# Kernel tuning notes

Measured on AMD Instinct MI355X. Metric: run time of the kernel, lower is better.

## Reference

```python
import jax, jax.numpy as jnp
import numpy as np

N = 100000
E = 1600000
IN_C, HID_C, OUT_C = 128, 64, 32


def _add_self_loops(edge_index, n):
    loops = jnp.arange(n, dtype=edge_index.dtype)
    src = jnp.concatenate([edge_index[0], loops])
    dst = jnp.concatenate([edge_index[1], loops])
    return src, dst


def _gcn_norm(src, dst, n):
    # symmetric normalization on A + I with unit edge weights
    deg = jax.ops.segment_sum(jnp.ones_like(dst, dtype=jnp.float32), dst, num_segments=n)
    dinv = jnp.where(deg > 0, jax.lax.rsqrt(deg), 0.0)
    return dinv[src] * dinv[dst]  # [E+N]


def _gcn_conv(x, src, dst, norm, W, b, n):
    h = x @ W                              # [N, out]
    msg = h[src] * norm[:, None]           # [E+N, out]  (dominant gather)
    out = jax.ops.segment_sum(msg, dst, num_segments=n)
    return out + b


def setup_inputs() -> dict:
    key = jax.random.key(0)
    k = jax.random.split(key, 6)
    x = jax.random.normal(k[0], (N, IN_C), dtype=jnp.float32)
    edge_index = jax.random.randint(k[1], (2, E), 0, N, dtype=jnp.int32)
    # Glorot-style init for GCN weights
    W1 = jax.random.normal(k[2], (IN_C, HID_C), dtype=jnp.float32) / np.sqrt(IN_C)
    b1 = jnp.zeros((HID_C,), dtype=jnp.float32)
    W2 = jax.random.normal(k[3], (HID_C, OUT_C), dtype=jnp.float32) / np.sqrt(HID_C)
    b2 = jnp.zeros((OUT_C,), dtype=jnp.float32)
    return {"x": x, "edge_index": edge_index, "W1": W1, "b1": b1, "W2": W2, "b2": b2}


def reference(x, edge_index, W1, b1, W2, b2):
    src, dst = _add_self_loops(edge_index, N)
    norm = _gcn_norm(src, dst, N)
    h = _gcn_conv(x, src, dst, norm, W1, b1, N)
    h = jax.nn.relu(h)
    # dropout p=0.2 is identity in eval mode
    out = _gcn_conv(h, src, dst, norm, W2, b2, N)
    return out
```

## Files before the change

kernel.cpp:

```cpp
#include <hip/hip_runtime.h>
#include <hip/hip_fp16.h>

#define N_NODES 100000
#define E_EDGES 1600000
#define IN_C 128
#define HID_C 64
#define OUT_C 32
#define BNODES 64
#define NBUCK ((N_NODES + BNODES - 1) / BNODES)
#define MAXB 2048
#define NCHUNK 256
#define CHUNK_E (E_EDGES / NCHUNK)
#define SCAN_N (NBUCK * NCHUNK)
#define SCAN_NB (SCAN_N / 256)

__device__ __forceinline__ int chunk_of_block(int b) { return (b & 7) * (NCHUNK / 8) + (b >> 3); }

__global__ __launch_bounds__(1024) void chunk_hist_kernel(const int* __restrict__ dst,
                                                          int* __restrict__ hist) {
    __shared__ int h[NBUCK];
    for (int i = threadIdx.x; i < NBUCK; i += 1024) h[i] = 0;
    __syncthreads();
    const int chunk = chunk_of_block(blockIdx.x);
    const int base = chunk * CHUNK_E;
    for (int j = threadIdx.x; j < CHUNK_E; j += 1024)
        atomicAdd(&h[dst[base + j] >> 6], 1);
    __syncthreads();
    for (int i = threadIdx.x; i < NBUCK; i += 1024)
        hist[i * NCHUNK + chunk] = h[i];
}

__global__ void scan1_kernel(int* __restrict__ data, int* __restrict__ bsums) {
    __shared__ int s[256];
    int i = blockIdx.x * 256 + threadIdx.x;
    int v = data[i];
    s[threadIdx.x] = v;
    __syncthreads();
    for (int off = 1; off < 256; off <<= 1) {
        int t = (threadIdx.x >= off) ? s[threadIdx.x - off] : 0;
        __syncthreads();
        s[threadIdx.x] += t;
        __syncthreads();
    }
    data[i] = s[threadIdx.x] - v;
    if (threadIdx.x == 255) bsums[blockIdx.x] = s[255];
}

__global__ __launch_bounds__(1024) void scan2_kernel(int* __restrict__ bsums) {
    __shared__ int s[1024];
    int total = 0;
    for (int base = 0; base < SCAN_NB; base += 1024) {
        int i = base + threadIdx.x;
        int v = (i < SCAN_NB) ? bsums[i] : 0;
        s[threadIdx.x] = v;
        __syncthreads();
        for (int off = 1; off < 1024; off <<= 1) {
            int t = (threadIdx.x >= off) ? s[threadIdx.x - off] : 0;
            __syncthreads();
            s[threadIdx.x] += t;
            __syncthreads();
        }
        if (i < SCAN_NB) bsums[i] = total + s[threadIdx.x] - v;
        total += s[1023];
        __syncthreads();
    }
}

__global__ __launch_bounds__(1024) void chunk_fill_kernel(const int* __restrict__ src,
                                                          const int* __restrict__ dst,
                                                          const int* __restrict__ hist,
                                                          const int* __restrict__ bsums,
                                                          unsigned* __restrict__ pairs) {
    __shared__ int cur[NBUCK];
    const int chunk = chunk_of_block(blockIdx.x);
    for (int i = threadIdx.x; i < NBUCK; i += 1024)
        cur[i] = hist[i * NCHUNK + chunk] + bsums[i];
    __syncthreads();
    const int base = chunk * CHUNK_E;
    for (int j = threadIdx.x; j < CHUNK_E; j += 1024) {
        int d = dst[base + j];
        int pos = atomicAdd(&cur[d >> 6], 1);
        pairs[pos] = ((unsigned)src[base + j] << 6) | (unsigned)(d & 63);
    }
}

__global__ __launch_bounds__(256) void bucket_sort_kernel(const int* __restrict__ hist,
                                                          const int* __restrict__ bsums,
                                                          unsigned* __restrict__ pairs,
                                                          int* __restrict__ row_ptr,
                                                          float* __restrict__ dinv) {
    __shared__ unsigned sp[MAXB];
    __shared__ int hcnt[BNODES], scn[BNODES], cur[BNODES];
    const int b = blockIdx.x;
    const int beg = hist[b * NCHUNK] + bsums[b];
    const int end = (b + 1 < NBUCK) ? hist[(b + 1) * NCHUNK] + bsums[b + 1] : E_EDGES;
    const int cnt = end - beg;
    if (threadIdx.x < BNODES) hcnt[threadIdx.x] = 0;
    __syncthreads();
    for (int j = threadIdx.x; j < cnt; j += 256) {
        unsigned p = pairs[beg + j];
        sp[j] = p;
        atomicAdd(&hcnt[p & 63], 1);
    }
    __syncthreads();
    if (threadIdx.x < BNODES) scn[threadIdx.x] = hcnt[threadIdx.x];
    __syncthreads();
    for (int off = 1; off < BNODES; off <<= 1) {
        int t = 0;
        if (threadIdx.x < BNODES && threadIdx.x >= off) t = scn[threadIdx.x - off];
        __syncthreads();
        if (threadIdx.x < BNODES) scn[threadIdx.x] += t;
        __syncthreads();
    }
    if (threadIdx.x < BNODES) {
        int ex = scn[threadIdx.x] - hcnt[threadIdx.x];
        cur[threadIdx.x] = ex;
        int node = b * BNODES + threadIdx.x;
        if (node < N_NODES) {
            row_ptr[node] = beg + ex;
            dinv[node] = rsqrtf((float)hcnt[threadIdx.x] + 1.0f);
        }
    }
    if (threadIdx.x == 0 && b == NBUCK - 1) row_ptr[N_NODES] = E_EDGES;
    __syncthreads();
    for (int j = threadIdx.x; j < cnt; j += 256) {
        unsigned p = sp[j];
        int pos = atomicAdd(&cur[p & 63], 1);
        pairs[beg + pos] = p >> 6;
    }
}

__global__ __launch_bounds__(256) void gemm1_kernel(const float* __restrict__ x,
                                                    const float* __restrict__ W1,
                                                    const float* __restrict__ dinv,
                                                    __half* __restrict__ hs) {
    __shared__ float sW[IN_C * HID_C];
    for (int i = threadIdx.x; i < IN_C * HID_C; i += 256) sW[i] = W1[i];
    __syncthreads();
    const int cg = (threadIdx.x & 7) * 8;
    const int row0 = blockIdx.x * 128 + (threadIdx.x >> 3) * 4;
    float acc[4][8];
#pragma unroll
    for (int r = 0; r < 4; ++r)
#pragma unroll
        for (int c = 0; c < 8; ++c) acc[r][c] = 0.f;

    int rr[4];
#pragma unroll
    for (int r = 0; r < 4; ++r) rr[r] = min(row0 + r, N_NODES - 1);

    const float4* x4 = (const float4*)x;
#pragma unroll 2
    for (int k4 = 0; k4 < IN_C / 4; ++k4) {
        float4 xv[4];
#pragma unroll
        for (int r = 0; r < 4; ++r) xv[r] = x4[(size_t)rr[r] * (IN_C / 4) + k4];
        float xs[4][4];
#pragma unroll
        for (int r = 0; r < 4; ++r) {
            xs[r][0] = xv[r].x; xs[r][1] = xv[r].y; xs[r][2] = xv[r].z; xs[r][3] = xv[r].w;
        }
#pragma unroll
        for (int kk = 0; kk < 4; ++kk) {
            const float4* wp = (const float4*)(sW + (k4 * 4 + kk) * HID_C + cg);
            float4 w0 = wp[0], w1 = wp[1];
            float wv[8] = {w0.x, w0.y, w0.z, w0.w, w1.x, w1.y, w1.z, w1.w};
#pragma unroll
            for (int r = 0; r < 4; ++r)
#pragma unroll
                for (int c = 0; c < 8; ++c)
                    acc[r][c] = fmaf(xs[r][kk], wv[c], acc[r][c]);
        }
    }
#pragma unroll
    for (int r = 0; r < 4; ++r) {
        int row = row0 + r;
        if (row < N_NODES) {
            float dv = dinv[row];
            union { float4 f; __half2 h[4]; } u;
#pragma unroll
            for (int q = 0; q < 4; ++q)
                u.h[q] = __floats2half2_rn(acc[r][2 * q] * dv, acc[r][2 * q + 1] * dv);
            *(float4*)(hs + (size_t)row * HID_C + cg) = u.f;
        }
    }
}

__global__ void agg1_kernel(const int* __restrict__ row_ptr, const int* __restrict__ col,
                            const __half2* __restrict__ hs2, const float* __restrict__ dinv,
                            const float* __restrict__ b1, __half2* __restrict__ h2h) {
    const int node = blockIdx.x * 8 + (threadIdx.x >> 5);
    const int c2 = threadIdx.x & 31;
    if (node >= N_NODES) return;
    const int beg = row_ptr[node], end = row_ptr[node + 1];
    float2 f = __half22float2(hs2[node * 32 + c2]);
    float ax = f.x, ay = f.y;
    int j = beg;
    for (; j + 7 < end; j += 8) {
        int s0 = col[j],     s1 = col[j + 1], s2 = col[j + 2], s3 = col[j + 3];
        int s4 = col[j + 4], s5 = col[j + 5], s6 = col[j + 6], s7 = col[j + 7];
        float2 v0 = __half22float2(hs2[s0 * 32 + c2]);
        float2 v1 = __half22float2(hs2[s1 * 32 + c2]);
        float2 v2 = __half22float2(hs2[s2 * 32 + c2]);
        float2 v3 = __half22float2(hs2[s3 * 32 + c2]);
        float2 v4 = __half22float2(hs2[s4 * 32 + c2]);
        float2 v5 = __half22float2(hs2[s5 * 32 + c2]);
        float2 v6 = __half22float2(hs2[s6 * 32 + c2]);
        float2 v7 = __half22float2(hs2[s7 * 32 + c2]);
        ax += ((v0.x + v1.x) + (v2.x + v3.x)) + ((v4.x + v5.x) + (v6.x + v7.x));
        ay += ((v0.y + v1.y) + (v2.y + v3.y)) + ((v4.y + v5.y) + (v6.y + v7.y));
    }
    for (; j + 1 < end; j += 2) {
        int s0 = col[j], s1 = col[j + 1];
        float2 v0 = __half22float2(hs2[s0 * 32 + c2]);
        float2 v1 = __half22float2(hs2[s1 * 32 + c2]);
        ax += v0.x + v1.x; ay += v0.y + v1.y;
    }
    if (j < end) {
        float2 v = __half22float2(hs2[col[j] * 32 + c2]);
        ax += v.x; ay += v.y;
    }
    float dv = dinv[node];
    float2 bb = ((const float2*)b1)[c2];
    h2h[node * 32 + c2] = __floats2half2_rn(fmaxf(dv * ax + bb.x, 0.f),
                                            fmaxf(dv * ay + bb.y, 0.f));
}

__global__ __launch_bounds__(256) void gemm2_kernel(const __half* __restrict__ h2h,
                                                    const float* __restrict__ W2,
                                                    const float* __restrict__ dinv,
                                                    __half* __restrict__ gs) {
    __shared__ float sW[HID_C * OUT_C];
    for (int i = threadIdx.x; i < HID_C * OUT_C; i += 256) sW[i] = W2[i];
    __syncthreads();
    const int cg = (threadIdx.x & 3) * 8;
    const int row0 = blockIdx.x * 128 + (threadIdx.x >> 2) * 2;
    float acc[2][8];
#pragma unroll
    for (int r = 0; r < 2; ++r)
#pragma unroll
        for (int c = 0; c < 8; ++c) acc[r][c] = 0.f;

    int rr[2];
#pragma unroll
    for (int r = 0; r < 2; ++r) rr[r] = min(row0 + r, N_NODES - 1);

    const float4* h4 = (const float4*)h2h;
    for (int k8 = 0; k8 < HID_C / 8; ++k8) {
        float xs[2][8];
#pragma unroll
        for (int r = 0; r < 2; ++r) {
            union { float4 f; __half2 h[4]; } u;
            u.f = h4[(size_t)rr[r] * (HID_C / 8) + k8];
#pragma unroll
            for (int q = 0; q < 4; ++q) {
                float2 v = __half22float2(u.h[q]);
                xs[r][2 * q] = v.x; xs[r][2 * q + 1] = v.y;
            }
        }
#pragma unroll
        for (int kk = 0; kk < 8; ++kk) {
            const float4* wp = (const float4*)(sW + (k8 * 8 + kk) * OUT_C + cg);
            float4 w0 = wp[0], w1 = wp[1];
            float wv[8] = {w0.x, w0.y, w0.z, w0.w, w1.x, w1.y, w1.z, w1.w};
#pragma unroll
            for (int r = 0; r < 2; ++r)
#pragma unroll
                for (int c = 0; c < 8; ++c)
                    acc[r][c] = fmaf(xs[r][kk], wv[c], acc[r][c]);
        }
    }
#pragma unroll
    for (int r = 0; r < 2; ++r) {
        int row = row0 + r;
        if (row < N_NODES) {
            float dv = dinv[row];
            union { float4 f; __half2 h[4]; } u;
#pragma unroll
            for (int q = 0; q < 4; ++q)
                u.h[q] = __floats2half2_rn(acc[r][2 * q] * dv, acc[r][2 * q + 1] * dv);
            *(float4*)(gs + (size_t)row * OUT_C + cg) = u.f;
        }
    }
}

__global__ void agg2_kernel(const int* __restrict__ row_ptr, const int* __restrict__ col,
                            const __half2* __restrict__ gs2, const float* __restrict__ dinv,
                            const float* __restrict__ b2, float* __restrict__ out) {
    const int node = blockIdx.x * 16 + (threadIdx.x >> 4);
    const int c2 = threadIdx.x & 15;
    if (node >= N_NODES) return;
    const int beg = row_ptr[node], end = row_ptr[node + 1];
    float2 f = __half22float2(gs2[node * 16 + c2]);
    float ax = f.x, ay = f.y;
    int j = beg;
    for (; j + 7 < end; j += 8) {
        int s0 = col[j],     s1 = col[j + 1], s2 = col[j + 2], s3 = col[j + 3];
        int s4 = col[j + 4], s5 = col[j + 5], s6 = col[j + 6], s7 = col[j + 7];
        float2 v0 = __half22float2(gs2[s0 * 16 + c2]);
        float2 v1 = __half22float2(gs2[s1 * 16 + c2]);
        float2 v2 = __half22float2(gs2[s2 * 16 + c2]);
        float2 v3 = __half22float2(gs2[s3 * 16 + c2]);
        float2 v4 = __half22float2(gs2[s4 * 16 + c2]);
        float2 v5 = __half22float2(gs2[s5 * 16 + c2]);
        float2 v6 = __half22float2(gs2[s6 * 16 + c2]);
        float2 v7 = __half22float2(gs2[s7 * 16 + c2]);
        ax += ((v0.x + v1.x) + (v2.x + v3.x)) + ((v4.x + v5.x) + (v6.x + v7.x));
        ay += ((v0.y + v1.y) + (v2.y + v3.y)) + ((v4.y + v5.y) + (v6.y + v7.y));
    }
    for (; j + 1 < end; j += 2) {
        int s0 = col[j], s1 = col[j + 1];
        float2 v0 = __half22float2(gs2[s0 * 16 + c2]);
        float2 v1 = __half22float2(gs2[s1 * 16 + c2]);
        ax += v0.x + v1.x; ay += v0.y + v1.y;
    }
    if (j < end) {
        float2 v = __half22float2(gs2[col[j] * 16 + c2]);
        ax += v.x; ay += v.y;
    }
    float dv = dinv[node];
    float2 bb = ((const float2*)b2)[c2];
    float2 o;
    o.x = dv * ax + bb.x;
    o.y = dv * ay + bb.y;
    ((float2*)out)[node * 16 + c2] = o;
}

extern "C" void kernel_launch(void* const* d_in, const int* in_sizes, int n_in,
                              void* d_out, int out_size, void* d_ws, size_t ws_size,
                              hipStream_t stream) {
    const float* x  = (const float*)d_in[0];
    const int*   ei = (const int*)d_in[1];
    const float* W1 = (const float*)d_in[2];
    const float* b1 = (const float*)d_in[3];
    const float* W2 = (const float*)d_in[4];
    const float* b2 = (const float*)d_in[5];
    float* out = (float*)d_out;

    const int* srcv = ei;
    const int* dstv = ei + E_EDGES;

    float* dinv  = (float*)d_ws;
    __half* hs   = (__half*)(dinv + N_NODES);
    __half* h2h  = hs + (size_t)N_NODES * HID_C;
    int* hist      = (int*)(h2h + (size_t)N_NODES * HID_C);
    int* bsums     = hist + SCAN_N;
    int* row_ptr   = bsums + SCAN_NB;
    unsigned* pairs = (unsigned*)(row_ptr + N_NODES + 1);
    __half* gs = hs;
    int* col = (int*)pairs;

    chunk_hist_kernel<<<NCHUNK, 1024, 0, stream>>>(dstv, hist);
    scan1_kernel<<<SCAN_NB, 256, 0, stream>>>(hist, bsums);
    scan2_kernel<<<1, 1024, 0, stream>>>(bsums);
    chunk_fill_kernel<<<NCHUNK, 1024, 0, stream>>>(srcv, dstv, hist, bsums, pairs);
    bucket_sort_kernel<<<NBUCK, 256, 0, stream>>>(hist, bsums, pairs, row_ptr, dinv);

    gemm1_kernel<<<(N_NODES + 127) / 128, 256, 0, stream>>>(x, W1, dinv, hs);
    agg1_kernel<<<(N_NODES + 7) / 8, 256, 0, stream>>>(row_ptr, col, (const __half2*)hs,
                                                       dinv, b1, (__half2*)h2h);

    gemm2_kernel<<<(N_NODES + 127) / 128, 256, 0, stream>>>(h2h, W2, dinv, gs);
    agg2_kernel<<<(N_NODES + 15) / 16, 256, 0, stream>>>(row_ptr, col, (const __half2*)gs,
                                                         dinv, b2, out);
}
```

Baseline: 144.9 us.

## Replace histogram-scan bucketing with fixed-capacity buckets and global atomic cursors

```diff
diff --git a/kernel.cpp b/kernel.cpp
--- a/kernel.cpp
+++ b/kernel.cpp
@@ -11,90 +11,56 @@
 #define MAXB 2048
 #define NCHUNK 256
 #define CHUNK_E (E_EDGES / NCHUNK)
-#define SCAN_N (NBUCK * NCHUNK)
-#define SCAN_NB (SCAN_N / 256)
 
 __device__ __forceinline__ int chunk_of_block(int b) { return (b & 7) * (NCHUNK / 8) + (b >> 3); }
 
-__global__ __launch_bounds__(1024) void chunk_hist_kernel(const int* __restrict__ dst,
-                                                          int* __restrict__ hist) {
+__global__ void zero_gcur_kernel(int* __restrict__ gcur) {
+    int i = blockIdx.x * 256 + threadIdx.x;
+    if (i < NBUCK) gcur[i] = 0;
+}
+
+__global__ __launch_bounds__(1024) void bucket_scatter_kernel(const int* __restrict__ src,
+                                                              const int* __restrict__ dst,
+                                                              int* __restrict__ gcur,
+                                                              unsigned* __restrict__ pairs) {
     __shared__ int h[NBUCK];
     for (int i = threadIdx.x; i < NBUCK; i += 1024) h[i] = 0;
     __syncthreads();
     const int chunk = chunk_of_block(blockIdx.x);
     const int base = chunk * CHUNK_E;
-    for (int j = threadIdx.x; j < CHUNK_E; j += 1024)
-        atomicAdd(&h[dst[base + j] >> 6], 1);
-    __syncthreads();
-    for (int i = threadIdx.x; i < NBUCK; i += 1024)
-        hist[i * NCHUNK + chunk] = h[i];
-}
-
-__global__ void scan1_kernel(int* __restrict__ data, int* __restrict__ bsums) {
-    __shared__ int s[256];
-    int i = blockIdx.x * 256 + threadIdx.x;
-    int v = data[i];
-    s[threadIdx.x] = v;
-    __syncthreads();
-    for (int off = 1; off < 256; off <<= 1) {
-        int t = (threadIdx.x >= off) ? s[threadIdx.x - off] : 0;
-        __syncthreads();
-        s[threadIdx.x] += t;
-        __syncthreads();
-    }
-    data[i] = s[threadIdx.x] - v;
-    if (threadIdx.x == 255) bsums[blockIdx.x] = s[255];
-}
-
-__global__ __launch_bounds__(1024) void scan2_kernel(int* __restrict__ bsums) {
-    __shared__ int s[1024];
-    int total = 0;
-    for (int base = 0; base < SCAN_NB; base += 1024) {
-        int i = base + threadIdx.x;
-        int v = (i < SCAN_NB) ? bsums[i] : 0;
-        s[threadIdx.x] = v;
-        __syncthreads();
-        for (int off = 1; off < 1024; off <<= 1) {
-            int t = (threadIdx.x >= off) ? s[threadIdx.x - off] : 0;
-            __syncthreads();
-            s[threadIdx.x] += t;
-            __syncthreads();
-        }
-        if (i < SCAN_NB) bsums[i] = total + s[threadIdx.x] - v;
-        total += s[1023];
-        __syncthreads();
-    }
-}
-
-__global__ __launch_bounds__(1024) void chunk_fill_kernel(const int* __restrict__ src,
-                                                          const int* __restrict__ dst,
-                                                          const int* __restrict__ hist,
-                                                          const int* __restrict__ bsums,
-                                                          unsigned* __restrict__ pairs) {
-    __shared__ int cur[NBUCK];
-    const int chunk = chunk_of_block(blockIdx.x);
-    for (int i = threadIdx.x; i < NBUCK; i += 1024)
-        cur[i] = hist[i * NCHUNK + chunk] + bsums[i];
-    __syncthreads();
-    const int base = chunk * CHUNK_E;
+    int dc[7];
+    int nj = 0;
     for (int j = threadIdx.x; j < CHUNK_E; j += 1024) {
         int d = dst[base + j];
-        int pos = atomicAdd(&cur[d >> 6], 1);
-        pairs[pos] = ((unsigned)src[base + j] << 6) | (unsigned)(d & 63);
-    }
-}
-
-__global__ __launch_bounds__(256) void bucket_sort_kernel(const int* __restrict__ hist,
-                                                          const int* __restrict__ bsums,
+        dc[nj++] = d;
+        atomicAdd(&h[d >> 6], 1);
+    }
+    __syncthreads();
+    for (int i = threadIdx.x; i < NBUCK; i += 1024) {
+        int c = h[i];
+        if (c > 0) h[i] = atomicAdd(&gcur[i], c);
+    }
+    __syncthreads();
+    nj = 0;
+    for (int j = threadIdx.x; j < CHUNK_E; j += 1024) {
+        int d = dc[nj++];
+        int pos = atomicAdd(&h[d >> 6], 1);
+        pairs[(unsigned)(d >> 6) * MAXB + (unsigned)pos] =
+            ((unsigned)src[base + j] << 6) | (unsigned)(d & 63);
+    }
+}
+
+__global__ __launch_bounds__(256) void bucket_sort_kernel(const int* __restrict__ gcur,
                                                           unsigned* __restrict__ pairs,
-                                                          int* __restrict__ row_ptr,
+                                                          int* __restrict__ row_beg,
+                                                          int* __restrict__ row_end,
                                                           float* __restrict__ dinv) {
     __shared__ unsigned sp[MAXB];
     __shared__ int hcnt[BNODES], scn[BNODES], cur[BNODES];
     const int b = blockIdx.x;
-    const int beg = hist[b * NCHUNK] + bsums[b];
-    const int end = (b + 1 < NBUCK) ? hist[(b + 1) * NCHUNK] + bsums[b + 1] : E_EDGES;
-    const int cnt = end - beg;
+    const int beg = b * MAXB;
+    int cnt = gcur[b];
+    if (cnt > MAXB) cnt = MAXB;
     if (threadIdx.x < BNODES) hcnt[threadIdx.x] = 0;
     __syncthreads();
     for (int j = threadIdx.x; j < cnt; j += 256) {
@@ -117,11 +83,11 @@
         cur[threadIdx.x] = ex;
         int node = b * BNODES + threadIdx.x;
         if (node < N_NODES) {
-            row_ptr[node] = beg + ex;
+            row_beg[node] = beg + ex;
+            row_end[node] = beg + ex + hcnt[threadIdx.x];
             dinv[node] = rsqrtf((float)hcnt[threadIdx.x] + 1.0f);
         }
     }
-    if (threadIdx.x == 0 && b == NBUCK - 1) row_ptr[N_NODES] = E_EDGES;
     __syncthreads();
     for (int j = threadIdx.x; j < cnt; j += 256) {
         unsigned p = sp[j];
@@ -186,13 +152,14 @@
     }
 }
 
-__global__ void agg1_kernel(const int* __restrict__ row_ptr, const int* __restrict__ col,
+__global__ void agg1_kernel(const int* __restrict__ row_beg, const int* __restrict__ row_end,
+                            const int* __restrict__ col,
                             const __half2* __restrict__ hs2, const float* __restrict__ dinv,
                             const float* __restrict__ b1, __half2* __restrict__ h2h) {
     const int node = blockIdx.x * 8 + (threadIdx.x >> 5);
     const int c2 = threadIdx.x & 31;
     if (node >= N_NODES) return;
-    const int beg = row_ptr[node], end = row_ptr[node + 1];
+    const int beg = row_beg[node], end = row_end[node];
     float2 f = __half22float2(hs2[node * 32 + c2]);
     float ax = f.x, ay = f.y;
     int j = beg;
@@ -284,13 +251,14 @@
     }
 }
 
-__global__ void agg2_kernel(const int* __restrict__ row_ptr, const int* __restrict__ col,
+__global__ void agg2_kernel(const int* __restrict__ row_beg, const int* __restrict__ row_end,
+                            const int* __restrict__ col,
                             const __half2* __restrict__ gs2, const float* __restrict__ dinv,
                             const float* __restrict__ b2, float* __restrict__ out) {
     const int node = blockIdx.x * 16 + (threadIdx.x >> 4);
     const int c2 = threadIdx.x & 15;
     if (node >= N_NODES) return;
-    const int beg = row_ptr[node], end = row_ptr[node + 1];
+    const int beg = row_beg[node], end = row_end[node];
     float2 f = __half22float2(gs2[node * 16 + c2]);
     float ax = f.x, ay = f.y;
     int j = beg;
@@ -343,24 +311,23 @@
     float* dinv  = (float*)d_ws;
     __half* hs   = (__half*)(dinv + N_NODES);
     __half* h2h  = hs + (size_t)N_NODES * HID_C;
-    int* hist      = (int*)(h2h + (size_t)N_NODES * HID_C);
-    int* bsums     = hist + SCAN_N;
-    int* row_ptr   = bsums + SCAN_NB;
-    unsigned* pairs = (unsigned*)(row_ptr + N_NODES + 1);
+    int* row_beg = (int*)(h2h + (size_t)N_NODES * HID_C);
+    int* row_end = row_beg + N_NODES;
+    int* gcur    = row_end + N_NODES;
+    unsigned* pairs = (unsigned*)(gcur + 1568);
     __half* gs = hs;
     int* col = (int*)pairs;
 
-    chunk_hist_kernel<<<NCHUNK, 1024, 0, stream>>>(dstv, hist);
-    scan1_kernel<<<SCAN_NB, 256, 0, stream>>>(hist, bsums);
-    scan2_kernel<<<1, 1024, 0, stream>>>(bsums);
-    chunk_fill_kernel<<<NCHUNK, 1024, 0, stream>>>(srcv, dstv, hist, bsums, pairs);
-    bucket_sort_kernel<<<NBUCK, 256, 0, stream>>>(hist, bsums, pairs, row_ptr, dinv);
+    zero_gcur_kernel<<<(NBUCK + 255) / 256, 256, 0, stream>>>(gcur);
+    bucket_scatter_kernel<<<NCHUNK, 1024, 0, stream>>>(srcv, dstv, gcur, pairs);
+    bucket_sort_kernel<<<NBUCK, 256, 0, stream>>>(gcur, pairs, row_beg, row_end, dinv);
 
     gemm1_kernel<<<(N_NODES + 127) / 128, 256, 0, stream>>>(x, W1, dinv, hs);
-    agg1_kernel<<<(N_NODES + 7) / 8, 256, 0, stream>>>(row_ptr, col, (const __half2*)hs,
-                                                       dinv, b1, (__half2*)h2h);
+    agg1_kernel<<<(N_NODES + 7) / 8, 256, 0, stream>>>(row_beg, row_end, col,
+                                                       (const __half2*)hs, dinv, b1,
+                                                       (__half2*)h2h);
 
     gemm2_kernel<<<(N_NODES + 127) / 128, 256, 0, stream>>>(h2h, W2, dinv, gs);
-    agg2_kernel<<<(N_NODES + 15) / 16, 256, 0, stream>>>(row_ptr, col, (const __half2*)gs,
-                                                         dinv, b2, out);
-}
+    agg2_kernel<<<(N_NODES + 15) / 16, 256, 0, stream>>>(row_beg, row_end, col,
+                                                         (const __half2*)gs, dinv, b2, out);
+}
```

New measurement: 144.3 us. No clear change (-0.4%).
